# Kernel tuning notes

Hardware: AMD Instinct MI355X
Metric: run time of the kernel (lower is better)

Reference implementation:

```python
import jax, jax.numpy as jnp
import numpy as np

NSIDE = 64
NLAT = 4 * NSIDE - 1        # 255 iso-latitude rings
NLON = 4 * NSIDE            # 256 = max pixels per ring
NPIX = 12 * NSIDE * NSIDE   # 49152 HEALPix pixels
LMAX = NLAT                 # 255
MMAX = NLON // 2 + 1        # 129
BATCH, CHAN = 8, 32


def _ring_geometry():
    # HEALPix ring scheme: ring r (0-based), 1-based i=r+1
    #  north cap i<nside: nph=4i, phi shift 0.5
    #  equatorial nside<=i<=3*nside: nph=4*nside, shift alternates {0,0.5}
    #  south cap: mirror of north cap
    nph = np.zeros(NLAT, np.int64)
    shift = np.zeros(NLAT, np.float64)
    for r in range(NLAT):
        i = r + 1
        if i < NSIDE:
            nph[r], shift[r] = 4 * i, 0.5
        elif i <= 3 * NSIDE:
            nph[r], shift[r] = 4 * NSIDE, 0.5 * ((i - NSIDE + 1) % 2)
        else:
            nph[r], shift[r] = 4 * (NLAT - r), 0.5
    offs = np.concatenate([[0], np.cumsum(nph)[:-1]])
    p = np.arange(NLON)
    mask = (p[None, :] < nph[:, None])                       # [nlat, nlon]
    idx = (offs[:, None] + p[None, :]) * mask                # padded -> 0
    phase = 2.0 * np.pi * (p[None, :] + shift[:, None]) / nph[:, None] * mask
    return idx.astype(np.int32), mask.astype(np.float32), phase.astype(np.float32)


def setup_inputs() -> dict:
    key = jax.random.key(0)
    k1, k2, k3 = jax.random.split(key, 3)
    idx, mask, phase = _ring_geometry()
    x = jax.random.normal(k1, (BATCH, CHAN, NPIX), jnp.float32)
    pct = jax.random.normal(k2, (MMAX, LMAX, NLAT), jnp.float32) * 0.1  # Legendre table stand-in
    w = jax.random.uniform(k3, (NLAT,), jnp.float32)                    # per-ring quadrature weights
    return {"x": x, "pct": pct, "w": w,
            "ring_index": jnp.asarray(idx),
            "ring_mask": jnp.asarray(mask),
            "phase": jnp.asarray(phase)}


def _healpix_rfft_real(x, ring_index, ring_mask, phase):
    # x: [..., npix] -> per-ring DFT coefficients as real pairs [..., nlat, mmax, 2]
    rings = x[..., ring_index] * ring_mask                 # [..., nlat, nlon]
    m = jnp.arange(MMAX, dtype=phase.dtype)
    ang = phase[:, :, None] * m                            # [nlat, nlon, mmax]
    fr = jnp.einsum('...kp,kpm->...km', rings, jnp.cos(ang))
    fi = -jnp.einsum('...kp,kpm->...km', rings, jnp.sin(ang))
    return jnp.stack([fr, fi], axis=-1)                    # n=2 is view_as_real axis


def reference(x, pct, w, ring_index, ring_mask, phase):
    # healpix ring rFFT, then Legendre contraction (einsum '...kmn,mlk->...lmn')
    f = _healpix_rfft_real(x, ring_index, ring_mask, phase)  # [..., nlat, mmax, 2]
    weights = pct * w                                        # [mmax, lmax, nlat]
    out = jnp.einsum('...kmn,mlk->...lmn', f, weights)       # [..., lmax, mmax, 2]
    return out
```

## Files before the change

kernel.cpp:

```cpp
#include <hip/hip_runtime.h>

#define NLAT 255
#define NLON 256
#define NPIX 49152
#define MMAX 129
#define MCS  258
#define NTBL 65
#define TROWS 264

typedef unsigned short ushort_t;
typedef __attribute__((ext_vector_type(8)))  short  bf16x8;
typedef __attribute__((ext_vector_type(4)))  short  short4v;
typedef __attribute__((ext_vector_type(16))) float  f32x16;
typedef __attribute__((ext_vector_type(4)))  float  float4v;

__device__ __forceinline__ ushort_t f2bf(float f) {
    union { float f; unsigned u; } v; v.f = f;
    unsigned r = v.u + 0x7FFFu + ((v.u >> 16) & 1u);
    return (ushort_t)(r >> 16);
}
__device__ __forceinline__ float bf2f(ushort_t h) {
    union { unsigned u; float f; } v; v.u = ((unsigned)h) << 16;
    return v.f;
}

__global__ __launch_bounds__(256) void prepK(const float* __restrict__ pct,
                                             const float* __restrict__ w,
                                             ushort_t* __restrict__ pctw) {
    const int m  = blockIdx.x;
    const int l0 = blockIdx.y * 32;
    const int t  = threadIdx.x;
    const float wk = (t < NLAT) ? w[t] : 0.f;
    for (int l = l0; l < l0 + 32; ++l) {
        float v = 0.f;
        if (l < NLAT && t < NLAT)
            v = pct[((size_t)m * NLAT + l) * NLAT + t] * wk;
        pctw[((size_t)m * 256 + l) * 256 + t] = f2bf(v);
    }
}

__global__ __launch_bounds__(256) void trigK(const float* __restrict__ phase,
                                             const float* __restrict__ mask,
                                             ushort_t* __restrict__ Ttab2) {
    const int tt  = blockIdx.x;
    const int mcs = blockIdx.y;
    const int p   = threadIdx.x;
    const int r   = (tt < 63) ? tt : (tt == 63 ? 63 : 64);
    float val = 0.f;
    if (mcs < MCS) {
        float ph = phase[r * NLON + p];
        float mk = mask[r * NLON + p];
        float fm = (float)(mcs >> 1);
        float s, c;
        __sincosf(ph * fm, &s, &c);
        val = (mcs & 1) ? (-s * mk) : (c * mk);
    }
    const int pl  = p & 63;
    const int swz = ((((pl >> 3) ^ mcs) & 7) << 3) | (pl & 7);
    Ttab2[(((size_t)tt * 4 + (p >> 6)) * TROWS + mcs) * 64 + swz] = f2bf(val);
}

__global__ __launch_bounds__(256, 3) void stageA(const float* __restrict__ x,
                                                 const int* __restrict__ ring_index,
                                                 const ushort_t* __restrict__ Ttab2,
                                                 ushort_t* __restrict__ f1) {
    __shared__ __align__(16) ushort_t Rs[64 * 72];
    __shared__ __align__(16) ushort_t Ts[TROWS * 64];

    const int b0 = blockIdx.x * 64;
    const int r  = blockIdx.y;
    const int i1 = r + 1;
    const int nph = (i1 < 64) ? 4 * i1 : (i1 <= 192 ? 256 : 4 * (256 - i1));
    const int tbl = (i1 < 64) ? r : (i1 <= 192 ? (63 + (((i1 - 63) & 1) ^ 1)) : 254 - r);
    const int base = ring_index[r * NLON];

    const int t    = threadIdx.x;
    const int lane = t & 63;
    const int wid  = t >> 6;
    const int wrow = wid >> 1, wcol = wid & 1;
    const int lg   = lane >> 5;
    const int lc   = lane & 31;

    f32x16 acc[5];
#pragma unroll
    for (int tau = 0; tau < 5; ++tau)
#pragma unroll
        for (int q = 0; q < 16; ++q) acc[tau][q] = 0.f;

    for (int pc = 0; pc < nph; pc += 64) {
        {
            const int p0 = (t & 15) * 4;
            const bool ok = (pc + p0) < nph;
#pragma unroll
            for (int pass = 0; pass < 4; ++pass) {
                int bc = (t >> 4) + pass * 16;
                float4v v = {0.f, 0.f, 0.f, 0.f};
                if (ok) v = *(const float4v*)(x + (size_t)(b0 + bc) * NPIX + base + pc + p0);
                short4v h;
                h[0] = (short)f2bf(v[0]); h[1] = (short)f2bf(v[1]);
                h[2] = (short)f2bf(v[2]); h[3] = (short)f2bf(v[3]);
                *(short4v*)(Rs + bc * 72 + p0) = h;
            }
        }
        {
            const ushort_t* slab = Ttab2 + ((size_t)tbl * 4 + (pc >> 6)) * (TROWS * 64);
            for (int s = wid; s < 33; s += 4) {
                __builtin_amdgcn_global_load_lds(
                    (const __attribute__((address_space(1))) void*)(slab + s * 512 + lane * 8),
                    (__attribute__((address_space(3))) void*)(Ts + s * 512),
                    16, 0, 0);
            }
        }
        __syncthreads();
#pragma unroll
        for (int ks = 0; ks < 4; ++ks) {
            bf16x8 a = *(const bf16x8*)(Rs + (wrow * 32 + lc) * 72 + ks * 16 + lg * 8);
            const int c = ks * 2 + lg;
#pragma unroll
            for (int tau = 0; tau < 5; ++tau) {
                int rr   = tau * 64 + wcol * 32 + lc;
                int trow = rr > (TROWS - 1) ? (TROWS - 1) : rr;
                bf16x8 b = *(const bf16x8*)(Ts + trow * 64 + ((c ^ (trow & 7)) << 3));
                acc[tau] = __builtin_amdgcn_mfma_f32_32x32x16_bf16(a, b, acc[tau], 0, 0, 0);
            }
        }
        __syncthreads();
    }

    ushort_t* Olds = Rs;
#pragma unroll
    for (int tau = 0; tau < 5; ++tau) {
        __syncthreads();
        {
            const int mcsl = wcol * 32 + lc;
#pragma unroll
            for (int q = 0; q < 16; ++q) {
                int bcl = wrow * 32 + 4 * lg + (q & 3) + 8 * (q >> 2);
                Olds[mcsl * 72 + bcl] = f2bf(acc[tau][q]);
            }
        }
        __syncthreads();
        {
            int row = t >> 2;
            int mcs = tau * 64 + row;
            if (mcs < MCS) {
                int m = mcs >> 1, n = mcs & 1;
                size_t gbase = ((size_t)m * NLAT + r) * 512 + n * 256 + b0 + (t & 3) * 16;
#pragma unroll
                for (int j = 0; j < 2; ++j) {
                    bf16x8 v = *(const bf16x8*)(Olds + row * 72 + (t & 3) * 16 + j * 8);
                    *(bf16x8*)(f1 + gbase + j * 8) = v;
                }
            }
        }
    }
}

__global__ __launch_bounds__(256) void transK(const ushort_t* __restrict__ f1,
                                              ushort_t* __restrict__ f1t, int m0) {
    __shared__ __align__(16) ushort_t T[64][72];
    const int m  = m0 + blockIdx.x;
    const int k0 = blockIdx.y * 64;
    const int b0 = blockIdx.z * 64;
    const int t  = threadIdx.x;
#pragma unroll
    for (int it = 0; it < 2; ++it) {
        int id = t + it * 256;
        int kk = id >> 3, ch = id & 7;
        int k  = k0 + kk;
        bf16x8 v = {0,0,0,0,0,0,0,0};
        if (k < NLAT)
            v = *(const bf16x8*)(f1 + ((size_t)m * NLAT + k) * 512 + b0 + ch * 8);
        *(bf16x8*)(&T[kk][ch * 8]) = v;
    }
    __syncthreads();
#pragma unroll
    for (int it = 0; it < 2; ++it) {
        int id  = t + it * 256;
        int bb  = id & 63, ch8 = id >> 6;
        bf16x8 v;
#pragma unroll
        for (int j = 0; j < 8; ++j) v[j] = T[ch8 * 8 + j][bb];
        *(bf16x8*)(f1t + ((size_t)m * 512 + b0 + bb) * 256 + k0 + ch8 * 8) = v;
    }
}

__global__ __launch_bounds__(256, 2) void stageB(const ushort_t* __restrict__ f1t,
                                                 const ushort_t* __restrict__ pctw,
                                                 ushort_t* __restrict__ otmp,
                                                 int mbase) {
    __shared__ __align__(16) ushort_t SB[30720];
    ushort_t* As = SB;
    ushort_t* Ws = SB + 10240;
    ushort_t* Es = SB;

    const int m   = mbase + (blockIdx.x >> 2);
    const int sub = blockIdx.x & 3;
    const int b2t = sub * 128;

    const int t     = threadIdx.x;
    const int lane  = t & 63;
    const int wid   = t >> 6;
    const int wrow  = wid >> 1, wlcol = wid & 1;
    const int lg    = lane >> 5, lc = lane & 31;

    f32x16 acc[2][4];
#pragma unroll
    for (int i = 0; i < 2; ++i)
#pragma unroll
        for (int j = 0; j < 4; ++j)
#pragma unroll
            for (int q = 0; q < 16; ++q) acc[i][j][q] = 0.f;

    auto fillA = [&](ushort_t* dst, int kc) {
#pragma unroll
        for (int pass = 0; pass < 2; ++pass) {
            int id  = t + pass * 256;
            int row = id >> 2, ch = id & 3;
            bf16x8 v = *(const bf16x8*)(f1t + ((size_t)m * 512 + b2t + row) * 256 + kc + ch * 8);
            *(bf16x8*)(dst + row * 40 + ch * 8) = v;
        }
    };
    auto fillW = [&](ushort_t* dst, int kc) {
#pragma unroll
        for (int pass = 0; pass < 4; ++pass) {
            int id  = t + pass * 256;
            int row = id >> 2, ch = id & 3;
            bf16x8 v = *(const bf16x8*)(pctw + ((size_t)m * 256 + row) * 256 + kc + ch * 8);
            *(bf16x8*)(dst + row * 40 + ch * 8) = v;
        }
    };

    fillA(As, 0);
    fillW(Ws, 0);
    __syncthreads();
    int buf = 0;
    for (int kc = 0; kc < 256; kc += 32, buf ^= 1) {
        if (kc + 32 < 256) {
            fillA(As + (buf ^ 1) * 5120, kc + 32);
            fillW(Ws + (buf ^ 1) * 10240, kc + 32);
        }
        const ushort_t* A = As + buf * 5120;
        const ushort_t* W = Ws + buf * 10240;
#pragma unroll
        for (int ks = 0; ks < 2; ++ks) {
            const int ko = ks * 16 + lg * 8;
            bf16x8 a0 = *(const bf16x8*)(A + (wrow * 64 + lc) * 40 + ko);
            bf16x8 a1 = *(const bf16x8*)(A + (wrow * 64 + 32 + lc) * 40 + ko);
#pragma unroll
            for (int jj = 0; jj < 4; ++jj) {
                bf16x8 b = *(const bf16x8*)(W + (wlcol * 128 + jj * 32 + lc) * 40 + ko);
                acc[0][jj] = __builtin_amdgcn_mfma_f32_32x32x16_bf16(a0, b, acc[0][jj], 0, 0, 0);
                acc[1][jj] = __builtin_amdgcn_mfma_f32_32x32x16_bf16(a1, b, acc[1][jj], 0, 0, 0);
            }
        }
        __syncthreads();
    }

#pragma unroll
    for (int h = 0; h < 2; ++h) {
        if (h) __syncthreads();
        if (wlcol == h) {
#pragma unroll
            for (int i = 0; i < 2; ++i)
#pragma unroll
                for (int jj = 0; jj < 4; ++jj)
#pragma unroll
                    for (int q = 0; q < 16; ++q) {
                        int bl = wrow * 64 + i * 32 + 4 * lg + (q & 3) + 8 * (q >> 2);
                        Es[bl * 136 + jj * 32 + lc] = f2bf(acc[i][jj][q]);
                    }
        }
        __syncthreads();
#pragma unroll
        for (int it = 0; it < 8; ++it) {
            int id  = t + it * 256;
            int row = id >> 4, ch = id & 15;
            bf16x8 v = *(const bf16x8*)(Es + row * 136 + ch * 8);
            *(bf16x8*)(otmp + (((size_t)m * 512 + b2t + row) << 8) + h * 128 + ch * 8) = v;
        }
    }
}

__global__ __launch_bounds__(256) void permuteK(const ushort_t* __restrict__ otmp,
                                                float* __restrict__ out) {
    __shared__ ushort_t L[MCS * 66];
    const int bc = blockIdx.x;
    const int l0 = blockIdx.y * 64;
    const int t  = threadIdx.x;
    const int ll = t & 63;
    const int l  = l0 + ll;
#pragma unroll 4
    for (int it = 0; it < 65; ++it) {
        int mn = (t >> 6) + it * 4;
        if (mn < MCS) {
            int mm = mn >> 1, n = mn & 1;
            ushort_t v = 0;
            if (l < NLAT)
                v = otmp[(((size_t)mm * 512 + n * 256 + bc) << 8) + l];
            L[mn * 66 + ll] = v;
        }
    }
    __syncthreads();
    for (int ll2 = 0; ll2 < 64; ++ll2) {
        int lo = l0 + ll2;
        if (lo >= NLAT) break;
        size_t rowb = ((size_t)bc * NLAT + lo) * MCS;
        out[rowb + t] = bf2f(L[t * 66 + ll2]);
        if (t < 2)
            out[rowb + 256 + t] = bf2f(L[(256 + t) * 66 + ll2]);
    }
}

extern "C" void kernel_launch(void* const* d_in, const int* in_sizes, int n_in,
                              void* d_out, int out_size, void* d_ws, size_t ws_size,
                              hipStream_t stream) {
    const float* x          = (const float*)d_in[0];
    const float* pct        = (const float*)d_in[1];
    const float* w          = (const float*)d_in[2];
    const int*   ring_index = (const int*)d_in[3];
    const float* ring_mask  = (const float*)d_in[4];
    const float* phase      = (const float*)d_in[5];
    float* out = (float*)d_out;

    char* wsb = (char*)d_ws;
    ushort_t* f1    = (ushort_t*)wsb;
    ushort_t* Ttab2 = (ushort_t*)(wsb + 33684480);
    ushort_t* f1t   = (ushort_t*)(wsb + 33552384);
    ushort_t* otmp  = (ushort_t*)wsb;
    ushort_t* pctw  = (ushort_t*)d_out;

    prepK   <<<dim3(MMAX, 8),     256, 0, stream>>>(pct, w, pctw);
    trigK   <<<dim3(NTBL, TROWS), 256, 0, stream>>>(phase, ring_mask, Ttab2);
    stageA  <<<dim3(4, NLAT),     256, 0, stream>>>(x, ring_index, Ttab2, f1);
    transK  <<<dim3(1, 4, 8),     256, 0, stream>>>(f1, f1t, 128);
    transK  <<<dim3(128, 4, 8),   256, 0, stream>>>(f1, f1t, 0);
    stageB  <<<dim3(256),         256, 0, stream>>>(f1t, pctw, otmp, 0);
    stageB  <<<dim3(260),         256, 0, stream>>>(f1t, pctw, otmp, 64);
    permuteK<<<dim3(256, 4),      256, 0, stream>>>(otmp, out);
}
```

Baseline: 142.8 us.

## Read trig table directly from global in stageA and merge split launches

The trig table is relaid out so each k-chunk of 8 columns is contiguous across rows. stageA now reads its B fragments straight from global/L2 instead of staging them in LDS, which removes the LDS slab and allows four blocks per CU. Workspace buffers are reassigned to the output buffer, so the split transK and stageB launches collapse into single launches. The trade-off is global-latency-bound B loads inside the MFMA loop, with no LDS reuse across waves.

```diff
diff --git a/kernel.cpp b/kernel.cpp
--- a/kernel.cpp
+++ b/kernel.cpp
@@ -41,7 +41,7 @@
 
 __global__ __launch_bounds__(256) void trigK(const float* __restrict__ phase,
                                              const float* __restrict__ mask,
-                                             ushort_t* __restrict__ Ttab2) {
+                                             ushort_t* __restrict__ Ttab3) {
     const int tt  = blockIdx.x;
     const int mcs = blockIdx.y;
     const int p   = threadIdx.x;
@@ -55,17 +55,15 @@
         __sincosf(ph * fm, &s, &c);
         val = (mcs & 1) ? (-s * mk) : (c * mk);
     }
-    const int pl  = p & 63;
-    const int swz = ((((pl >> 3) ^ mcs) & 7) << 3) | (pl & 7);
-    Ttab2[(((size_t)tt * 4 + (p >> 6)) * TROWS + mcs) * 64 + swz] = f2bf(val);
-}
-
-__global__ __launch_bounds__(256, 3) void stageA(const float* __restrict__ x,
+    const int pcc = p >> 6, c = (p >> 3) & 7, j = p & 7;
+    Ttab3[((((size_t)tt * 4 + pcc) * 8 + c) * TROWS + mcs) * 8 + j] = f2bf(val);
+}
+
+__global__ __launch_bounds__(256, 4) void stageA(const float* __restrict__ x,
                                                  const int* __restrict__ ring_index,
-                                                 const ushort_t* __restrict__ Ttab2,
+                                                 const ushort_t* __restrict__ Ttab3,
                                                  ushort_t* __restrict__ f1) {
     __shared__ __align__(16) ushort_t Rs[64 * 72];
-    __shared__ __align__(16) ushort_t Ts[TROWS * 64];
 
     const int b0 = blockIdx.x * 64;
     const int r  = blockIdx.y;
@@ -102,25 +100,17 @@
                 *(short4v*)(Rs + bc * 72 + p0) = h;
             }
         }
-        {
-            const ushort_t* slab = Ttab2 + ((size_t)tbl * 4 + (pc >> 6)) * (TROWS * 64);
-            for (int s = wid; s < 33; s += 4) {
-                __builtin_amdgcn_global_load_lds(
-                    (const __attribute__((address_space(1))) void*)(slab + s * 512 + lane * 8),
-                    (__attribute__((address_space(3))) void*)(Ts + s * 512),
-                    16, 0, 0);
-            }
-        }
-        __syncthreads();
+        __syncthreads();
+        const ushort_t* slab = Ttab3 + (size_t)(tbl * 4 + (pc >> 6)) * (8 * TROWS * 8);
 #pragma unroll
         for (int ks = 0; ks < 4; ++ks) {
             bf16x8 a = *(const bf16x8*)(Rs + (wrow * 32 + lc) * 72 + ks * 16 + lg * 8);
-            const int c = ks * 2 + lg;
+            const ushort_t* bcol = slab + (size_t)(ks * 2 + lg) * (TROWS * 8);
 #pragma unroll
             for (int tau = 0; tau < 5; ++tau) {
                 int rr   = tau * 64 + wcol * 32 + lc;
                 int trow = rr > (TROWS - 1) ? (TROWS - 1) : rr;
-                bf16x8 b = *(const bf16x8*)(Ts + trow * 64 + ((c ^ (trow & 7)) << 3));
+                bf16x8 b = *(const bf16x8*)(bcol + trow * 8);
                 acc[tau] = __builtin_amdgcn_mfma_f32_32x32x16_bf16(a, b, acc[tau], 0, 0, 0);
             }
         }
@@ -157,9 +147,9 @@
 }
 
 __global__ __launch_bounds__(256) void transK(const ushort_t* __restrict__ f1,
-                                              ushort_t* __restrict__ f1t, int m0) {
+                                              ushort_t* __restrict__ f1t) {
     __shared__ __align__(16) ushort_t T[64][72];
-    const int m  = m0 + blockIdx.x;
+    const int m  = blockIdx.x;
     const int k0 = blockIdx.y * 64;
     const int b0 = blockIdx.z * 64;
     const int t  = threadIdx.x;
@@ -187,14 +177,13 @@
 
 __global__ __launch_bounds__(256, 2) void stageB(const ushort_t* __restrict__ f1t,
                                                  const ushort_t* __restrict__ pctw,
-                                                 ushort_t* __restrict__ otmp,
-                                                 int mbase) {
+                                                 ushort_t* __restrict__ otmp) {
     __shared__ __align__(16) ushort_t SB[30720];
     ushort_t* As = SB;
     ushort_t* Ws = SB + 10240;
     ushort_t* Es = SB;
 
-    const int m   = mbase + (blockIdx.x >> 2);
+    const int m   = blockIdx.x >> 2;
     const int sub = blockIdx.x & 3;
     const int b2t = sub * 128;
 
@@ -324,18 +313,17 @@
     float* out = (float*)d_out;
 
     char* wsb = (char*)d_ws;
-    ushort_t* f1    = (ushort_t*)wsb;
-    ushort_t* Ttab2 = (ushort_t*)(wsb + 33684480);
-    ushort_t* f1t   = (ushort_t*)(wsb + 33552384);
+    char* ob  = (char*)d_out;
     ushort_t* otmp  = (ushort_t*)wsb;
-    ushort_t* pctw  = (ushort_t*)d_out;
+    ushort_t* f1    = (ushort_t*)(wsb + 33552384);
+    ushort_t* f1t   = (ushort_t*)ob;
+    ushort_t* pctw  = (ushort_t*)(ob + 33816576);
+    ushort_t* Ttab3 = (ushort_t*)(ob + 50724864);
 
     prepK   <<<dim3(MMAX, 8),     256, 0, stream>>>(pct, w, pctw);
-    trigK   <<<dim3(NTBL, TROWS), 256, 0, stream>>>(phase, ring_mask, Ttab2);
-    stageA  <<<dim3(4, NLAT),     256, 0, stream>>>(x, ring_index, Ttab2, f1);
-    transK  <<<dim3(1, 4, 8),     256, 0, stream>>>(f1, f1t, 128);
-    transK  <<<dim3(128, 4, 8),   256, 0, stream>>>(f1, f1t, 0);
-    stageB  <<<dim3(256),         256, 0, stream>>>(f1t, pctw, otmp, 0);
-    stageB  <<<dim3(260),         256, 0, stream>>>(f1t, pctw, otmp, 64);
+    trigK   <<<dim3(NTBL, TROWS), 256, 0, stream>>>(phase, ring_mask, Ttab3);
+    stageA  <<<dim3(4, NLAT),     256, 0, stream>>>(x, ring_index, Ttab3, f1);
+    transK  <<<dim3(MMAX, 4, 8),  256, 0, stream>>>(f1, f1t);
+    stageB  <<<dim3(4 * MMAX),    256, 0, stream>>>(f1t, pctw, otmp);
     permuteK<<<dim3(256, 4),      256, 0, stream>>>(otmp, out);
 }
```

Measured after the change: 154.7 us. 8.3% more time.
